# Kernel optimization log

Measured on AMD Instinct MI355X. Metric: run time of the kernel, lower is better.

Reference implementation:

```python
import jax, jax.numpy as jnp
import numpy as np
from jax import lax

B, T_ENCO, N_INP, N_HID, T_DECO = 1024, 128, 128, 256, 24


def _lin(x, W, b):
    return x @ W.T + b


def _lstm_cell(x, h, c, Wih, Whh, bih, bhh):
    # PyTorch LSTMCell gate order: input, forget, cell(g), output
    g = x @ Wih.T + bih + h @ Whh.T + bhh
    i, f, gg, o = jnp.split(g, 4, axis=-1)
    c2 = jax.nn.sigmoid(f) * c + jax.nn.sigmoid(i) * jnp.tanh(gg)
    return jax.nn.sigmoid(o) * jnp.tanh(c2), c2


def setup_inputs() -> dict:
    key = jax.random.key(0)
    ks = iter(jax.random.split(key, 48))
    def w(shape, s=0.05):
        return jax.random.normal(next(ks), shape, jnp.float32) * s
    m = N_HID
    return {
        "input_p_q": jax.random.normal(next(ks), (B, T_ENCO, N_INP), jnp.float32),
        "label_p": jax.random.normal(next(ks), (B, T_DECO), jnp.float32),
        "Ue_W": w((m, T_ENCO)), "Ue_b": w((m,)),
        "Ue2_W": w((m, N_INP)), "Ue2_b": w((m,)),
        "We_W": w((m, 2 * N_HID)), "We_b": w((m,)),
        "Ve_W": w((1, m)), "Ve_b": w((1,)),
        "Ud_W": w((N_HID, N_HID)), "Ud_b": w((N_HID,)),
        "Wd_W": w((N_HID, 2 * N_HID)), "Wd_b": w((N_HID,)),
        "Vd_W": w((1, N_HID)), "Vd_b": w((1,)),
        "enc_Wih": w((4 * N_HID, N_INP)), "enc_Whh": w((4 * N_HID, N_HID)),
        "enc_bih": w((4 * N_HID,)), "enc_bhh": w((4 * N_HID,)),
        "mid_Wih": w((4 * N_HID, N_HID)), "mid_Whh": w((4 * N_HID, N_HID)),
        "mid_bih": w((4 * N_HID,)), "mid_bhh": w((4 * N_HID,)),
        "dec_Wih": w((4 * N_HID, N_HID)), "dec_Whh": w((4 * N_HID, N_HID)),
        "dec_bih": w((4 * N_HID,)), "dec_bhh": w((4 * N_HID,)),
        "reg_W": w((1, N_HID)), "reg_b": w((1,)),
    }


def reference(input_p_q, label_p, Ue_W, Ue_b, Ue2_W, Ue2_b, We_W, We_b, Ve_W, Ve_b,
              Ud_W, Ud_b, Wd_W, Wd_b, Vd_W, Vd_b,
              enc_Wih, enc_Whh, enc_bih, enc_bhh,
              mid_Wih, mid_Whh, mid_bih, mid_bhh,
              dec_Wih, dec_Whh, dec_bih, dec_bhh,
              reg_W, reg_b):
    bsz = input_p_q.shape[0]
    inputs = input_p_q[:, :T_ENCO, :]                       # [B, T, n_inp]
    # Ue(inputs.transpose(1,2)) is loop-invariant: [B, n_inp, m]
    ue_x = _lin(jnp.swapaxes(inputs, 1, 2), Ue_W, Ue_b)
    z = jnp.zeros((bsz, N_HID), inputs.dtype)

    # --- spatial-attention encoder (LSTMCell over time) ---
    def enc_step(carry, x_i):                               # x_i: [B, n_inp]
        h, c = carry
        hc = _lin(jnp.concatenate([h, c], axis=1), We_W, We_b)[:, None, :]
        xi = _lin(x_i, Ue2_W, Ue2_b)[:, None, :]
        score = _lin(jnp.tanh(hc + ue_x + xi), Ve_W, Ve_b)[..., 0]  # [B, n_inp]
        a = jax.nn.softmax(score, axis=1)
        h2, c2 = _lstm_cell(x_i * a, h, c, enc_Wih, enc_Whh, enc_bih, enc_bhh)
        return (h2, c2), h2

    _, enc_hs = lax.scan(enc_step, (z, z), jnp.swapaxes(inputs, 0, 1))  # [T, B, H]

    # --- middle single-layer LSTM (zero init state) ---
    def mid_step(carry, x_t):
        h, c = carry
        h2, c2 = _lstm_cell(x_t, h, c, mid_Wih, mid_Whh, mid_bih, mid_bhh)
        return (h2, c2), h2

    _, mid = lax.scan(mid_step, (z, z), enc_hs)
    mid = jnp.swapaxes(mid, 0, 1)                            # [B, T, H]
    ud_mid = _lin(mid, Ud_W, Ud_b)                           # loop-invariant

    # --- temporal-attention decoder (note: raw (un-softmaxed) scores used in bmm,
    #     matching the original code) ---
    def dec_step(carry, _):
        hi, ci = carry
        wd = _lin(jnp.concatenate([hi, ci], axis=1), Wd_W, Wd_b)[:, None, :]
        t = _lin(jnp.tanh(wd + ud_mid), Vd_W, Vd_b)[..., 0]  # [B, T]
        dec_in = jnp.einsum('bt,bth->bh', t, mid)
        hi2, ci2 = _lstm_cell(dec_in, hi, ci, dec_Wih, dec_Whh, dec_bih, dec_bhh)
        return (hi2, ci2), hi2

    _, dec = lax.scan(dec_step, (z, z), None, length=T_DECO + 6)
    dec = jnp.swapaxes(dec, 0, 1)                            # [B, T_deco+6, H]
    out = _lin(dec, reg_W, reg_b)[..., 0]                    # [B, T_deco+6]
    return out[:, -T_DECO:]
```

## Files before the change

### kernel.cpp

```cpp
#include <hip/hip_runtime.h>


#define B_   1024
#define T_   128
#define NI_  128
#define H_   256
#define H4_  1024
#define TD_  24
#define DS_  30
#define BB   4
#define TB   1024

typedef _Float16 hf_t;
typedef _Float16 half8  __attribute__((ext_vector_type(8)));
typedef _Float16 half2v __attribute__((ext_vector_type(2)));

__device__ __forceinline__ float sigm(float x) {
    return __builtin_amdgcn_rcpf(1.0f + __expf(-x));
}
__device__ __forceinline__ float tanh_f(float x) {
    float e = __expf(2.0f * x);
    return 1.0f - 2.0f * __builtin_amdgcn_rcpf(e + 1.0f);
}
__device__ __forceinline__ float fdot2f(half2v a, half2v b, float c) {
#if __has_builtin(__builtin_amdgcn_fdot2)
    return __builtin_amdgcn_fdot2(a, b, c, false);
#else
    return fmaf((float)a.x, (float)b.x, fmaf((float)a.y, (float)b.y, c));
#endif
}
__device__ __forceinline__ float dot8h(half8 w, half8 x, float acc) {
    acc = fdot2f(__builtin_shufflevector(w, w, 0, 1), __builtin_shufflevector(x, x, 0, 1), acc);
    acc = fdot2f(__builtin_shufflevector(w, w, 2, 3), __builtin_shufflevector(x, x, 2, 3), acc);
    acc = fdot2f(__builtin_shufflevector(w, w, 4, 5), __builtin_shufflevector(x, x, 4, 5), acc);
    acc = fdot2f(__builtin_shufflevector(w, w, 6, 7), __builtin_shufflevector(x, x, 6, 7), acc);
    return acc;
}
__device__ __forceinline__ hf_t ld_h(const hf_t* p) { return *p; }
__device__ __forceinline__ void st_h(hf_t v, hf_t* p) { *p = v; }

#define W_WE    0u
#define W_UE2   131072u
#define W_EWIH  163840u
#define W_EWHH  294912u
#define W_MWIH  557056u
#define W_MWHH  819200u
#define W_DWIH  1081344u
#define W_DWHH  1343488u
#define W_WD    1605632u
#define W_UD    1736704u
#define SCR_A   2097152u
#define SCR_B   35651584u

__global__ void convw_kernel(const float* __restrict__ sWE, const float* __restrict__ sUE2,
                             const float* __restrict__ sEI, const float* __restrict__ sEH,
                             const float* __restrict__ sMI, const float* __restrict__ sMH,
                             const float* __restrict__ sDI, const float* __restrict__ sDH,
                             const float* __restrict__ sWD, const float* __restrict__ sUD,
                             hf_t* __restrict__ dst) {
    const int gtid = blockIdx.x * blockDim.x + threadIdx.x;
    const int gs   = gridDim.x * blockDim.x;
    for (int n = gtid; n < 131072; n += gs) {
        int e = n & 7, q = n >> 3, k = q & 255, c = q >> 8, kq = c >> 4, i = c & 15;
        dst[W_WE + n] = (hf_t)sWE[k * 512 + kq * 128 + i * 8 + e];
    }
    for (int n = gtid; n < 32768; n += gs) {
        int e = n & 7, q = n >> 3, k = q & 255, c = q >> 8, kq = c >> 2, i = c & 3;
        dst[W_UE2 + n] = (hf_t)sUE2[k * 128 + kq * 32 + i * 8 + e];
    }
    for (int n = gtid; n < 131072; n += gs) {
        int e = n & 7, q = n >> 3, o = q & 1023, i = q >> 10;
        dst[W_EWIH + n] = (hf_t)sEI[o * 128 + i * 8 + e];
    }
    for (int n = gtid; n < 262144; n += gs) {
        int e = n & 7, q = n >> 3, o = q & 1023, i = q >> 10;
        int s = o * 256 + i * 8 + e;
        dst[W_EWHH + n] = (hf_t)sEH[s];
        dst[W_MWIH + n] = (hf_t)sMI[s];
        dst[W_MWHH + n] = (hf_t)sMH[s];
        dst[W_DWIH + n] = (hf_t)sDI[s];
        dst[W_DWHH + n] = (hf_t)sDH[s];
    }
    for (int n = gtid; n < 131072; n += gs) {
        int e = n & 7, q = n >> 3, k = q & 255, c = q >> 8, kq = c >> 4, i = c & 15;
        dst[W_WD + n] = (hf_t)sWD[k * 512 + kq * 128 + i * 8 + e];
    }
    for (int n = gtid; n < 65536; n += gs)
        dst[W_UD + n] = (hf_t)sUD[n];
}

#define O_HC    0
#define O_CF    1024
#define O_HM    2048
#define O_CMF   2560
#define O_XRAW  3584
#define O_XH    4096
#define O_XG    4352
#define O_HCXI  4608
#define O_SPART 5632
#define O_SBUF  6656
#define O_GBUF  7168
#define O_DINH  11264
#define O_HF    11776
#define O_VES   12800
#define O_VDS   13056

__global__ __launch_bounds__(TB, 4) void dsrnn_kernel(
    const float* __restrict__ inp,
    const float* __restrict__ UeW,  const float* __restrict__ Ueb,
    const float* __restrict__ Ue2b,
    const float* __restrict__ Web,
    const float* __restrict__ VeW,  const float* __restrict__ Veb,
    const float* __restrict__ Udb,
    const float* __restrict__ Wdb,
    const float* __restrict__ VdW,  const float* __restrict__ Vdb,
    const float* __restrict__ ebih, const float* __restrict__ ebhh,
    const float* __restrict__ mbih, const float* __restrict__ mbhh,
    const float* __restrict__ dbih, const float* __restrict__ dbhh,
    const float* __restrict__ rW,   const float* __restrict__ rb,
    const hf_t* __restrict__ wb,
    hf_t* __restrict__ scrA,
    hf_t* __restrict__ scrB,
    float* __restrict__ out)
{
    __shared__ float sm[16384];
    const int tid = threadIdx.x;
    const int b0  = blockIdx.x * BB;

    hf_t*  hc   = (hf_t*)(sm + O_HC);
    float* cf   = sm + O_CF;
    hf_t*  hm   = (hf_t*)(sm + O_HM);
    float* cmf  = sm + O_CMF;
    float* xraw = sm + O_XRAW;
    hf_t*  xh   = (hf_t*)(sm + O_XH);
    hf_t*  xg   = (hf_t*)(sm + O_XG);
    float* hcxi = sm + O_HCXI;
    float* spart= sm + O_SPART;
    float* sbuf = sm + O_SBUF;
    float* gbuf = sm + O_GBUF;
    hf_t*  dinh = (hf_t*)(sm + O_DINH);
    float* hful = sm + O_HF;
    float* ves  = sm + O_VES;
    float* vds  = sm + O_VDS;

    {
        const int j = tid & 127, kq8 = tid >> 7;
        for (int b = 0; b < BB; ++b) {
            __syncthreads();
            const float* Xg = inp + (size_t)(b0 + b) * T_ * NI_;
            for (int i = tid; i < T_ * NI_; i += TB) sm[i] = Xg[i];
            __syncthreads();
            hf_t* ub = scrA + (size_t)(b0 + b) * H_ * NI_;
            for (int k = kq8 * 32; k < kq8 * 32 + 32; ++k) {
                const float* wrow = UeW + (size_t)k * T_;
                float acc = Ueb[k];
#pragma unroll 4
                for (int t = 0; t < T_; ++t) acc = fmaf(wrow[t], sm[t * NI_ + j], acc);
                st_h((hf_t)acc, ub + (size_t)k * NI_ + j);
            }
        }
    }
    __syncthreads();
    for (int i = tid; i < 3584; i += TB) sm[i] = 0.0f;
    if (tid < 256) { ves[tid] = VeW[tid]; vds[tid] = VdW[tid]; }
    __syncthreads();

    for (int t = 0; t < T_; ++t) {
        if (tid < 512) {
            const int b = tid >> 7, j = tid & 127;
            float v = inp[((size_t)(b0 + b) * T_ + t) * NI_ + j];
            xraw[b * NI_ + j] = v;
            xh[b * NI_ + j]   = (hf_t)v;
        }
        __syncthreads();

        {
            const int k = tid & 255, kq = tid >> 8;
            const half8* wWE = (const half8*)(wb + W_WE)  + (size_t)(kq * 16) * 256 + k;
            const half8* wU2 = (const half8*)(wb + W_UE2) + (size_t)(kq * 4)  * 256 + k;
            float a0 = 0.f, a1 = 0.f, a2 = 0.f, a3 = 0.f;
#pragma unroll 8
            for (int i = 0; i < 16; ++i) {
                half8 w = wWE[(size_t)i * 256];
                a0 = dot8h(w, *(const half8*)&hc[0 * 512 + kq * 128 + i * 8], a0);
                a1 = dot8h(w, *(const half8*)&hc[1 * 512 + kq * 128 + i * 8], a1);
                a2 = dot8h(w, *(const half8*)&hc[2 * 512 + kq * 128 + i * 8], a2);
                a3 = dot8h(w, *(const half8*)&hc[3 * 512 + kq * 128 + i * 8], a3);
            }
#pragma unroll
            for (int i = 0; i < 4; ++i) {
                half8 w = wU2[(size_t)i * 256];
                a0 = dot8h(w, *(const half8*)&xh[0 * 128 + kq * 32 + i * 8], a0);
                a1 = dot8h(w, *(const half8*)&xh[1 * 128 + kq * 32 + i * 8], a1);
                a2 = dot8h(w, *(const half8*)&xh[2 * 128 + kq * 32 + i * 8], a2);
                a3 = dot8h(w, *(const half8*)&xh[3 * 128 + kq * 32 + i * 8], a3);
            }
            gbuf[kq * 1024 + 0 * 256 + k] = a0;
            gbuf[kq * 1024 + 1 * 256 + k] = a1;
            gbuf[kq * 1024 + 2 * 256 + k] = a2;
            gbuf[kq * 1024 + 3 * 256 + k] = a3;
        }
        __syncthreads();
        {
            const int b = tid >> 8, k = tid & 255;
            hcxi[b * 256 + k] = gbuf[b * 256 + k] + gbuf[1024 + b * 256 + k]
                              + gbuf[2048 + b * 256 + k] + gbuf[3072 + b * 256 + k]
                              + Web[k] + Ue2b[k];
        }
        __syncthreads();

        {
            const int b = tid >> 8, r = tid & 255, kh = r >> 7, j = r & 127;
            const hf_t* up = scrA + ((size_t)(b0 + b) * 256 + kh * 128) * 128 + j;
            const float* hx = hcxi + b * 256 + kh * 128;
            const float* vw = ves + kh * 128;
            float acc = kh ? 0.f : Veb[0];
#pragma unroll 8
            for (int k2 = 0; k2 < 128; ++k2) {
                float u = (float)ld_h(up + (size_t)k2 * 128);
                acc = fmaf(vw[k2], tanh_f(hx[k2] + u), acc);
            }
            spart[tid] = acc;
        }
        __syncthreads();

        if (tid < 256) {
            const int b = tid >> 6, lane = tid & 63;
            const int base = b << 8;
            float sA = spart[base + lane]      + spart[base + 128 + lane];
            float sB = spart[base + 64 + lane] + spart[base + 192 + lane];
            float m = fmaxf(sA, sB);
            for (int d = 1; d < 64; d <<= 1) m = fmaxf(m, __shfl_xor(m, d));
            float eA = __expf(sA - m), eB = __expf(sB - m);
            float ssum = eA + eB;
            for (int d = 1; d < 64; d <<= 1) ssum += __shfl_xor(ssum, d);
            float inv = 1.0f / ssum;
            xg[b * NI_ + lane]      = (hf_t)(xraw[b * NI_ + lane] * eA * inv);
            xg[b * NI_ + lane + 64] = (hf_t)(xraw[b * NI_ + lane + 64] * eB * inv);
        }
        __syncthreads();

        {
            const int o = tid;
            const half8* wih = (const half8*)(wb + W_EWIH) + o;
            const half8* whh = (const half8*)(wb + W_EWHH) + o;
            float bias = ebih[o] + ebhh[o];
            float a0 = bias, a1 = bias, a2 = bias, a3 = bias;
#pragma unroll 8
            for (int i = 0; i < 16; ++i) {
                half8 w = wih[(size_t)i * 1024];
                a0 = dot8h(w, *(const half8*)&xg[0 * 128 + i * 8], a0);
                a1 = dot8h(w, *(const half8*)&xg[1 * 128 + i * 8], a1);
                a2 = dot8h(w, *(const half8*)&xg[2 * 128 + i * 8], a2);
                a3 = dot8h(w, *(const half8*)&xg[3 * 128 + i * 8], a3);
            }
#pragma unroll 8
            for (int i = 0; i < 32; ++i) {
                half8 w = whh[(size_t)i * 1024];
                a0 = dot8h(w, *(const half8*)&hc[0 * 512 + i * 8], a0);
                a1 = dot8h(w, *(const half8*)&hc[1 * 512 + i * 8], a1);
                a2 = dot8h(w, *(const half8*)&hc[2 * 512 + i * 8], a2);
                a3 = dot8h(w, *(const half8*)&hc[3 * 512 + i * 8], a3);
            }
            gbuf[0 * 1024 + o] = a0; gbuf[1 * 1024 + o] = a1;
            gbuf[2 * 1024 + o] = a2; gbuf[3 * 1024 + o] = a3;
        }
        __syncthreads();

        {
            const int b = tid >> 8, k = tid & 255;
            float gi = gbuf[b * H4_ + k];
            float gf = gbuf[b * H4_ + H_ + k];
            float gg = gbuf[b * H4_ + 2 * H_ + k];
            float go = gbuf[b * H4_ + 3 * H_ + k];
            float c2 = sigm(gf) * cf[b * H_ + k] + sigm(gi) * tanh_f(gg);
            float h2 = sigm(go) * tanh_f(c2);
            cf[b * H_ + k] = c2;
            hc[b * 512 + k]       = (hf_t)h2;
            hc[b * 512 + 256 + k] = (hf_t)c2;
        }
        __syncthreads();

        {
            const int o = tid;
            const half8* wih = (const half8*)(wb + W_MWIH) + o;
            const half8* whh = (const half8*)(wb + W_MWHH) + o;
            float bias = mbih[o] + mbhh[o];
            float a0 = bias, a1 = bias, a2 = bias, a3 = bias;
#pragma unroll 8
            for (int i = 0; i < 32; ++i) {
                half8 w = wih[(size_t)i * 1024];
                a0 = dot8h(w, *(const half8*)&hc[0 * 512 + i * 8], a0);
                a1 = dot8h(w, *(const half8*)&hc[1 * 512 + i * 8], a1);
                a2 = dot8h(w, *(const half8*)&hc[2 * 512 + i * 8], a2);
                a3 = dot8h(w, *(const half8*)&hc[3 * 512 + i * 8], a3);
            }
#pragma unroll 8
            for (int i = 0; i < 32; ++i) {
                half8 w = whh[(size_t)i * 1024];
                a0 = dot8h(w, *(const half8*)&hm[0 * 256 + i * 8], a0);
                a1 = dot8h(w, *(const half8*)&hm[1 * 256 + i * 8], a1);
                a2 = dot8h(w, *(const half8*)&hm[2 * 256 + i * 8], a2);
                a3 = dot8h(w, *(const half8*)&hm[3 * 256 + i * 8], a3);
            }
            gbuf[0 * 1024 + o] = a0; gbuf[1 * 1024 + o] = a1;
            gbuf[2 * 1024 + o] = a2; gbuf[3 * 1024 + o] = a3;
        }
        __syncthreads();

        {
            const int b = tid >> 8, k = tid & 255;
            float gi = gbuf[b * H4_ + k];
            float gf = gbuf[b * H4_ + H_ + k];
            float gg = gbuf[b * H4_ + 2 * H_ + k];
            float go = gbuf[b * H4_ + 3 * H_ + k];
            float c2 = sigm(gf) * cmf[b * H_ + k] + sigm(gi) * tanh_f(gg);
            float h2 = sigm(go) * tanh_f(c2);
            cmf[b * H_ + k] = c2;
            hm[b * 256 + k] = (hf_t)h2;
            scrB[((size_t)(b0 + b) * T_ + t) * H_ + k] = (hf_t)h2;
        }
        __syncthreads();
    }

    {
        const int b = tid >> 8, r = tid & 255, oh = r >> 7, tt = r & 127;
        const half8* mrow = (const half8*)(scrB + ((size_t)(b0 + b) * T_ + tt) * H_);
        half8 m[32];
#pragma unroll
        for (int i = 0; i < 32; ++i) m[i] = mrow[i];
        const half8* udw = (const half8*)(wb + W_UD);
        for (int o2 = 0; o2 < 128; ++o2) {
            const int o = oh * 128 + o2;
            const half8* ur = udw + (size_t)o * 32;
            float acc = Udb[o];
#pragma unroll 8
            for (int i = 0; i < 32; ++i) acc = dot8h(ur[i], m[i], acc);
            st_h((hf_t)acc, scrA + ((size_t)(b0 + b) * 256 + o) * 128 + tt);
        }
    }
    __syncthreads();
    for (int i = tid; i < 2048; i += TB) sm[i] = 0.0f;
    __syncthreads();

    for (int s = 0; s < DS_; ++s) {
        {
            const int k = tid & 255, kq = tid >> 8;
            const half8* wWD = (const half8*)(wb + W_WD) + (size_t)(kq * 16) * 256 + k;
            float a0 = 0.f, a1 = 0.f, a2 = 0.f, a3 = 0.f;
#pragma unroll 8
            for (int i = 0; i < 16; ++i) {
                half8 w = wWD[(size_t)i * 256];
                a0 = dot8h(w, *(const half8*)&hc[0 * 512 + kq * 128 + i * 8], a0);
                a1 = dot8h(w, *(const half8*)&hc[1 * 512 + kq * 128 + i * 8], a1);
                a2 = dot8h(w, *(const half8*)&hc[2 * 512 + kq * 128 + i * 8], a2);
                a3 = dot8h(w, *(const half8*)&hc[3 * 512 + kq * 128 + i * 8], a3);
            }
            gbuf[kq * 1024 + 0 * 256 + k] = a0;
            gbuf[kq * 1024 + 1 * 256 + k] = a1;
            gbuf[kq * 1024 + 2 * 256 + k] = a2;
            gbuf[kq * 1024 + 3 * 256 + k] = a3;
        }
        __syncthreads();
        {
            const int b = tid >> 8, k = tid & 255;
            hcxi[b * 256 + k] = gbuf[b * 256 + k] + gbuf[1024 + b * 256 + k]
                              + gbuf[2048 + b * 256 + k] + gbuf[3072 + b * 256 + k]
                              + Wdb[k];
        }
        __syncthreads();

        {
            const int b = tid >> 8, r = tid & 255, kh = r >> 7, j = r & 127;
            const hf_t* up = scrA + ((size_t)(b0 + b) * 256 + kh * 128) * 128 + j;
            const float* hx = hcxi + b * 256 + kh * 128;
            const float* vw = vds + kh * 128;
            float acc = kh ? 0.f : Vdb[0];
#pragma unroll 8
            for (int k2 = 0; k2 < 128; ++k2) {
                float u = (float)ld_h(up + (size_t)k2 * 128);
                acc = fmaf(vw[k2], tanh_f(hx[k2] + u), acc);
            }
            spart[tid] = acc;
        }
        __syncthreads();
        if (tid < 512) {
            const int b = tid >> 7, j = tid & 127;
            sbuf[b * T_ + j] = spart[(b << 8) + j] + spart[(b << 8) + 128 + j];
        }
        __syncthreads();

        {
            const int b = tid >> 8, h = tid & 255;
            const hf_t* mp = scrB + (size_t)(b0 + b) * T_ * H_ + h;
            float acc = 0.0f;
            for (int j = 0; j < T_; ++j)
                acc = fmaf(sbuf[b * T_ + j], (float)mp[(size_t)j * H_], acc);
            dinh[b * 256 + h] = (hf_t)acc;
        }
        __syncthreads();

        {
            const int o = tid;
            const half8* wih = (const half8*)(wb + W_DWIH) + o;
            const half8* whh = (const half8*)(wb + W_DWHH) + o;
            float bias = dbih[o] + dbhh[o];
            float a0 = bias, a1 = bias, a2 = bias, a3 = bias;
#pragma unroll 8
            for (int i = 0; i < 32; ++i) {
                half8 w = wih[(size_t)i * 1024];
                a0 = dot8h(w, *(const half8*)&dinh[0 * 256 + i * 8], a0);
                a1 = dot8h(w, *(const half8*)&dinh[1 * 256 + i * 8], a1);
                a2 = dot8h(w, *(const half8*)&dinh[2 * 256 + i * 8], a2);
                a3 = dot8h(w, *(const half8*)&dinh[3 * 256 + i * 8], a3);
            }
#pragma unroll 8
            for (int i = 0; i < 32; ++i) {
                half8 w = whh[(size_t)i * 1024];
                a0 = dot8h(w, *(const half8*)&hc[0 * 512 + i * 8], a0);
                a1 = dot8h(w, *(const half8*)&hc[1 * 512 + i * 8], a1);
                a2 = dot8h(w, *(const half8*)&hc[2 * 512 + i * 8], a2);
                a3 = dot8h(w, *(const half8*)&hc[3 * 512 + i * 8], a3);
            }
            gbuf[0 * 1024 + o] = a0; gbuf[1 * 1024 + o] = a1;
            gbuf[2 * 1024 + o] = a2; gbuf[3 * 1024 + o] = a3;
        }
        __syncthreads();

        {
            const int b = tid >> 8, k = tid & 255;
            float gi = gbuf[b * H4_ + k];
            float gf = gbuf[b * H4_ + H_ + k];
            float gg = gbuf[b * H4_ + 2 * H_ + k];
            float go = gbuf[b * H4_ + 3 * H_ + k];
            float c2 = sigm(gf) * cf[b * H_ + k] + sigm(gi) * tanh_f(gg);
            float h2 = sigm(go) * tanh_f(c2);
            cf[b * H_ + k] = c2;
            hc[b * 512 + k]       = (hf_t)h2;
            hc[b * 512 + 256 + k] = (hf_t)c2;
            hful[b * H_ + k] = h2;
        }
        __syncthreads();

        if (s >= 6 && tid < 256) {
            const int b = tid >> 6, lane = tid & 63;
            float p = rW[lane]       * hful[b * H_ + lane]
                    + rW[lane + 64]  * hful[b * H_ + lane + 64]
                    + rW[lane + 128] * hful[b * H_ + lane + 128]
                    + rW[lane + 192] * hful[b * H_ + lane + 192];
            for (int d = 1; d < 64; d <<= 1) p += __shfl_xor(p, d);
            if (lane == 0) out[(size_t)(b0 + b) * TD_ + (s - 6)] = p + rb[0];
        }
        __syncthreads();
    }
}

extern "C" void kernel_launch(void* const* d_in, const int* in_sizes, int n_in,
                              void* d_out, int out_size, void* d_ws, size_t ws_size,
                              hipStream_t stream) {
    const float* inp  = (const float*)d_in[0];
    const float* UeW  = (const float*)d_in[2];
    const float* Ueb  = (const float*)d_in[3];
    const float* Ue2W = (const float*)d_in[4];
    const float* Ue2b = (const float*)d_in[5];
    const float* WeW  = (const float*)d_in[6];
    const float* Web  = (const float*)d_in[7];
    const float* VeW  = (const float*)d_in[8];
    const float* Veb  = (const float*)d_in[9];
    const float* UdW  = (const float*)d_in[10];
    const float* Udb  = (const float*)d_in[11];
    const float* WdW  = (const float*)d_in[12];
    const float* Wdb  = (const float*)d_in[13];
    const float* VdW  = (const float*)d_in[14];
    const float* Vdb  = (const float*)d_in[15];
    const float* eWih = (const float*)d_in[16];
    const float* eWhh = (const float*)d_in[17];
    const float* ebih = (const float*)d_in[18];
    const float* ebhh = (const float*)d_in[19];
    const float* mWih = (const float*)d_in[20];
    const float* mWhh = (const float*)d_in[21];
    const float* mbih = (const float*)d_in[22];
    const float* mbhh = (const float*)d_in[23];
    const float* dWih = (const float*)d_in[24];
    const float* dWhh = (const float*)d_in[25];
    const float* dbih = (const float*)d_in[26];
    const float* dbhh = (const float*)d_in[27];
    const float* rW   = (const float*)d_in[28];
    const float* rb   = (const float*)d_in[29];

    hf_t* wsb  = (hf_t*)d_ws;
    hf_t* scrA = wsb + SCR_A;
    hf_t* scrB = wsb + SCR_B;

    convw_kernel<<<512, 256, 0, stream>>>(WeW, Ue2W, eWih, eWhh, mWih, mWhh,
                                          dWih, dWhh, WdW, UdW, wsb);

    dsrnn_kernel<<<B_ / BB, TB, 0, stream>>>(
        inp, UeW, Ueb, Ue2b, Web, VeW, Veb, Udb, Wdb, VdW, Vdb,
        ebih, ebhh, mbih, mbhh, dbih, dbhh, rW, rb,
        wsb, scrA, scrB, (float*)d_out);
}
```

Before: 12.63 ms.

## Keep attention projections in registers instead of re-reading global scratch each step

The encoder's Ue projection and the decoder's Ud projection used to be written to global scratch as fp16 and reloaded every timestep inside the tanh-score loops. The Ue projection is now computed straight into per-thread half8 registers (16 vectors), and the score work is repartitioned so each thread reduces over its own 32 k values for all 4 batch rows, with a cross-group sum added in the softmax stage. The Ud projection is stored transposed so each thread can preload its 128 values once into registers before the decoder loop. This removes the repeated global or L2 loads of 128-strided elements per step, at the cost of 32 extra half8 registers per thread, which may cause spilling at 1024 threads per block.

```diff
diff --git a/kernel.cpp b/kernel.cpp
--- a/kernel.cpp
+++ b/kernel.cpp
@@ -36,8 +36,6 @@
     acc = fdot2f(__builtin_shufflevector(w, w, 6, 7), __builtin_shufflevector(x, x, 6, 7), acc);
     return acc;
 }
-__device__ __forceinline__ hf_t ld_h(const hf_t* p) { return *p; }
-__device__ __forceinline__ void st_h(hf_t v, hf_t* p) { *p = v; }
 
 #define W_WE    0u
 #define W_UE2   131072u
@@ -143,20 +141,28 @@
     float* ves  = sm + O_VES;
     float* vds  = sm + O_VDS;
 
+    half8 u1v[16];
     {
-        const int j = tid & 127, kq8 = tid >> 7;
+        const int j = tid & 127, kg = tid >> 7;
+#pragma unroll
         for (int b = 0; b < BB; ++b) {
             __syncthreads();
             const float* Xg = inp + (size_t)(b0 + b) * T_ * NI_;
             for (int i = tid; i < T_ * NI_; i += TB) sm[i] = Xg[i];
             __syncthreads();
-            hf_t* ub = scrA + (size_t)(b0 + b) * H_ * NI_;
-            for (int k = kq8 * 32; k < kq8 * 32 + 32; ++k) {
-                const float* wrow = UeW + (size_t)k * T_;
-                float acc = Ueb[k];
+#pragma unroll
+            for (int idx = 0; idx < 4; ++idx) {
+                half8 v;
+#pragma unroll
+                for (int e = 0; e < 8; ++e) {
+                    const int k = (kg << 5) + idx * 8 + e;
+                    const float* wrow = UeW + (size_t)k * T_;
+                    float acc = Ueb[k];
 #pragma unroll 4
-                for (int t = 0; t < T_; ++t) acc = fmaf(wrow[t], sm[t * NI_ + j], acc);
-                st_h((hf_t)acc, ub + (size_t)k * NI_ + j);
+                    for (int t = 0; t < T_; ++t) acc = fmaf(wrow[t], sm[t * NI_ + j], acc);
+                    v[e] = (hf_t)acc;
+                }
+                u1v[b * 4 + idx] = v;
             }
         }
     }
@@ -210,25 +216,31 @@
         __syncthreads();
 
         {
-            const int b = tid >> 8, r = tid & 255, kh = r >> 7, j = r & 127;
-            const hf_t* up = scrA + ((size_t)(b0 + b) * 256 + kh * 128) * 128 + j;
-            const float* hx = hcxi + b * 256 + kh * 128;
-            const float* vw = ves + kh * 128;
-            float acc = kh ? 0.f : Veb[0];
-#pragma unroll 8
-            for (int k2 = 0; k2 < 128; ++k2) {
-                float u = (float)ld_h(up + (size_t)k2 * 128);
-                acc = fmaf(vw[k2], tanh_f(hx[k2] + u), acc);
-            }
-            spart[tid] = acc;
+            const int j = tid & 127, kg = tid >> 7;
+#pragma unroll
+            for (int b = 0; b < BB; ++b) {
+                float a = 0.f;
+#pragma unroll
+                for (int idx = 0; idx < 4; ++idx) {
+#pragma unroll
+                    for (int e = 0; e < 8; ++e) {
+                        const int k = (kg << 5) + idx * 8 + e;
+                        a = fmaf(ves[k], tanh_f(hcxi[b * 256 + k] + (float)u1v[b * 4 + idx][e]), a);
+                    }
+                }
+                gbuf[(b * 8 + kg) * 128 + j] = a;
+            }
         }
         __syncthreads();
 
         if (tid < 256) {
             const int b = tid >> 6, lane = tid & 63;
-            const int base = b << 8;
-            float sA = spart[base + lane]      + spart[base + 128 + lane];
-            float sB = spart[base + 64 + lane] + spart[base + 192 + lane];
+            float sA = 0.f, sB = 0.f;
+#pragma unroll
+            for (int kg = 0; kg < 8; ++kg) {
+                sA += gbuf[(b * 8 + kg) * 128 + lane];
+                sB += gbuf[(b * 8 + kg) * 128 + lane + 64];
+            }
             float m = fmaxf(sA, sB);
             for (int d = 1; d < 64; d <<= 1) m = fmaxf(m, __shfl_xor(m, d));
             float eA = __expf(sA - m), eB = __expf(sB - m);
@@ -330,16 +342,30 @@
 #pragma unroll
         for (int i = 0; i < 32; ++i) m[i] = mrow[i];
         const half8* udw = (const half8*)(wb + W_UD);
-        for (int o2 = 0; o2 < 128; ++o2) {
-            const int o = oh * 128 + o2;
-            const half8* ur = udw + (size_t)o * 32;
-            float acc = Udb[o];
-#pragma unroll 8
-            for (int i = 0; i < 32; ++i) acc = dot8h(ur[i], m[i], acc);
-            st_h((hf_t)acc, scrA + ((size_t)(b0 + b) * 256 + o) * 128 + tt);
+        hf_t* dst = scrA + ((size_t)(b0 + b) * 128 + tt) * 256 + oh * 128;
+        for (int idx = 0; idx < 16; ++idx) {
+            half8 v;
+#pragma unroll
+            for (int e = 0; e < 8; ++e) {
+                const int o = oh * 128 + idx * 8 + e;
+                const half8* ur = udw + (size_t)o * 32;
+                float acc = Udb[o];
+#pragma unroll 8
+                for (int i = 0; i < 32; ++i) acc = dot8h(ur[i], m[i], acc);
+                v[e] = (hf_t)acc;
+            }
+            ((half8*)dst)[idx] = v;
         }
     }
     __syncthreads();
+
+    half8 u2v[16];
+    {
+        const int b = tid >> 8, r = tid & 255, kh = r >> 7, j = r & 127;
+        const half8* up = (const half8*)(scrA + ((size_t)(b0 + b) * 128 + j) * 256 + kh * 128);
+#pragma unroll
+        for (int idx = 0; idx < 16; ++idx) u2v[idx] = up[idx];
+    }
     for (int i = tid; i < 2048; i += TB) sm[i] = 0.0f;
     __syncthreads();
 
@@ -371,22 +397,24 @@
         __syncthreads();
 
         {
-            const int b = tid >> 8, r = tid & 255, kh = r >> 7, j = r & 127;
-            const hf_t* up = scrA + ((size_t)(b0 + b) * 256 + kh * 128) * 128 + j;
+            const int b = tid >> 8, r = tid & 255, kh = r >> 7;
             const float* hx = hcxi + b * 256 + kh * 128;
             const float* vw = vds + kh * 128;
-            float acc = kh ? 0.f : Vdb[0];
-#pragma unroll 8
-            for (int k2 = 0; k2 < 128; ++k2) {
-                float u = (float)ld_h(up + (size_t)k2 * 128);
-                acc = fmaf(vw[k2], tanh_f(hx[k2] + u), acc);
+            float acc = 0.f;
+#pragma unroll
+            for (int idx = 0; idx < 16; ++idx) {
+#pragma unroll
+                for (int e = 0; e < 8; ++e) {
+                    const int k2 = idx * 8 + e;
+                    acc = fmaf(vw[k2], tanh_f(hx[k2] + (float)u2v[idx][e]), acc);
+                }
             }
             spart[tid] = acc;
         }
         __syncthreads();
         if (tid < 512) {
             const int b = tid >> 7, j = tid & 127;
-            sbuf[b * T_ + j] = spart[(b << 8) + j] + spart[(b << 8) + 128 + j];
+            sbuf[b * T_ + j] = spart[(b << 8) + j] + spart[(b << 8) + 128 + j] + Vdb[0];
         }
         __syncthreads();
 
```

New measurement: 16.86 ms. 1.33x slower.
